# Kernel tuning notes

Hardware: AMD Instinct MI355X
Metric: run time of the kernel (lower is better)

## Reference

```python
import jax, jax.numpy as jnp
import numpy as np

B, F, L, H, D = 8, 256, 2048, 8, 32
INV_SQRT_2PI = 1.0 / np.sqrt(2.0 * 3.1415926)


def setup_inputs() -> dict:
    key = jax.random.key(0)
    k0, k1, k2 = jax.random.split(key, 3)
    # xavier-normal-ish scale for the projections
    scale = np.sqrt(2.0 / (F + H * D)).astype(np.float32)
    return {
        "inputs": jax.random.normal(k0, (B, F, L), dtype=jnp.float32),
        "Wq": jax.random.normal(k1, (F, H * D), dtype=jnp.float32) * scale,
        "bq": jnp.zeros((H * D,), dtype=jnp.float32),
        "Wk": jax.random.normal(k2, (F, H * D), dtype=jnp.float32) * scale,
        "bk": jnp.zeros((H * D,), dtype=jnp.float32),
        "prior_mean": jnp.zeros((1,), dtype=jnp.float32),
        "prior_std": jnp.ones((1,), dtype=jnp.float32),
    }


def reference(inputs, Wq, bq, Wk, bk, prior_mean, prior_std):
    # inputs: [B, F, L] -> x: [B, L, F]
    x = jnp.transpose(inputs, (0, 2, 1))
    Lx = x.shape[1]
    # projections, reshaped to per-head: [B, L, H, D]
    q = (x @ Wq + bq).reshape(B, Lx, H, D)
    k = (x @ Wk + bk).reshape(B, Lx, H, D)
    # distance matrix: dist[i, j] = j - i
    idx = jnp.arange(Lx, dtype=jnp.float32)
    dist = idx[None, :] - idx[:, None]                      # [L, L]
    # gaussian positional prior
    prior = (INV_SQRT_2PI / prior_std[0]) * jnp.exp(
        -0.5 * (dist - prior_mean[0]) ** 2 / prior_std[0] ** 2
    )                                                       # [L, L]
    # scaled QK^T per head, modulated by prior, softmax over keys
    att = jnp.einsum("blhd,bmhd->bhlm", q, k) * (float(D) ** -0.5)
    att = att * prior[None, None, :, :]
    att = jax.nn.softmax(att, axis=-1)                      # [B, H, L, L]
    # distance-weighted reduction over keys -> [B, H, L]
    out = jnp.einsum("bhlm,lm->bhl", att, dist)
    # [B, L, H] to match torch split/cat layout
    return jnp.transpose(out, (0, 2, 1))
```

## Files before the change

### kernel.cpp

```cpp
#include <hip/hip_runtime.h>
#include <hip/hip_bf16.h>
#include <math.h>

#define B 8
#define F 256
#define L 2048
#define H 8
#define D 32
#define HD 256
#define W 6
#define HALO 8
#define KST 264
#define QSTF 132

typedef __attribute__((ext_vector_type(8))) short bf16x8;
typedef __attribute__((ext_vector_type(4))) float f32x4;

__device__ __forceinline__ unsigned short f2bf_fast(float f) {
    union { float f; unsigned u; } v; v.f = f;
    return (unsigned short)((v.u + 0x8000u) >> 16);
}
__device__ __forceinline__ float bf2f(unsigned u16) {
    union { unsigned u; float f; } v; v.u = u16 << 16;
    return v.f;
}

__global__ __launch_bounds__(256) void prep_w_kernel(
    const float* __restrict__ Wq, const float* __restrict__ Wk,
    unsigned short* __restrict__ Wt)
{
    __shared__ unsigned short Ts[64][72];
    const int t   = threadIdx.x;
    const int sel = blockIdx.x >> 2;
    const int c0  = (blockIdx.x & 3) * 64;
    const int r0  = blockIdx.y * 64;
    const float* __restrict__ src = sel ? Wk : Wq;
    unsigned short* __restrict__ dst = Wt + (size_t)sel * HD * F;

    #pragma unroll
    for (int rr = 0; rr < 4; ++rr) {
        int r = rr * 16 + (t >> 4);
        int cb = (t & 15) * 4;
        float4 v = *(const float4*)&src[(size_t)(r0 + r) * HD + c0 + cb];
        Ts[r][cb + 0] = f2bf_fast(v.x);
        Ts[r][cb + 1] = f2bf_fast(v.y);
        Ts[r][cb + 2] = f2bf_fast(v.z);
        Ts[r][cb + 3] = f2bf_fast(v.w);
    }
    __syncthreads();
    const int c = t >> 2;
    #pragma unroll
    for (int half = 0; half < 2; ++half) {
        int ch = (t & 3) + half * 4;
        unsigned short tmp[8];
        #pragma unroll
        for (int j = 0; j < 8; ++j) tmp[j] = Ts[ch * 8 + j][c];
        *(uint4*)&dst[(size_t)(c0 + c) * F + r0 + ch * 8] = *(const uint4*)tmp;
    }
}

__global__ __launch_bounds__(256, 1) void fused_kernel(
    const float* __restrict__ x, const unsigned short* __restrict__ Wt,
    const float* __restrict__ bq, const float* __restrict__ bk,
    const float* __restrict__ pmean, const float* __restrict__ pstd,
    float* __restrict__ out)
{
    __shared__ uint4 smem4[5280];
    unsigned short* Xs = (unsigned short*)smem4;
    float*          Qs = (float*)smem4;
    unsigned short* Ks = (unsigned short*)(smem4 + 2640);

    const int t    = threadIdx.x;
    const int l0   = blockIdx.x * 64;
    const int b    = blockIdx.y;
    const int lane = t & 63, wv = t >> 6;
    const int lm   = lane & 15, quad = lane >> 4;

    const float* __restrict__ xb = x + (size_t)b * F * L;
    #pragma unroll
    for (int i = 0; i < 20; ++i) {
        int idx = i * 256 + t;
        int lp  = idx % 80;
        int fg  = idx / 80;
        int m   = l0 - HALO + lp;
        m = min(max(m, 0), L - 1);
        unsigned p0, p1;
        {
            float v0 = xb[(size_t)(4 * fg + 0) * L + m];
            float v1 = xb[(size_t)(4 * fg + 1) * L + m];
            p0 = ((__float_as_uint(v0) + 0x8000u) >> 16) |
                 (((__float_as_uint(v1) + 0x8000u) >> 16) << 16);
            float v2 = xb[(size_t)(4 * fg + 2) * L + m];
            float v3 = xb[(size_t)(4 * fg + 3) * L + m];
            p1 = ((__float_as_uint(v2) + 0x8000u) >> 16) |
                 (((__float_as_uint(v3) + 0x8000u) >> 16) << 16);
        }
        uint2 pk; pk.x = p0; pk.y = p1;
        *(uint2*)&Xs[lp * KST + 4 * fg] = pk;
    }
    __syncthreads();

    bf16x8 af[5][8];
    #pragma unroll
    for (int mt = 0; mt < 5; ++mt)
        #pragma unroll
        for (int ks = 0; ks < 8; ++ks)
            af[mt][ks] = *(const bf16x8*)&Xs[(mt * 16 + lm) * KST + ks * 32 + quad * 8];
    __syncthreads();

    #pragma unroll
    for (int nt = 0; nt < 8; ++nt) {
        const int hdq = wv * 128 + nt * 16 + lm;
        const int sel = hdq >> 8;
        const int hd  = hdq & 255;
        const unsigned short* Brow = Wt + ((size_t)sel * HD + hd) * F;
        f32x4 acc[5];
        #pragma unroll
        for (int mt = 0; mt < 5; ++mt) acc[mt] = (f32x4){0.f, 0.f, 0.f, 0.f};
        #pragma unroll
        for (int ks = 0; ks < 8; ++ks) {
            bf16x8 bfr = *(const bf16x8*)&Brow[ks * 32 + quad * 8];
            #pragma unroll
            for (int mt = 0; mt < 5; ++mt)
                acc[mt] = __builtin_amdgcn_mfma_f32_16x16x32_bf16(
                    af[mt][ks], bfr, acc[mt], 0, 0, 0);
        }
        float bv = sel ? bk[hd] : bq[hd];
        if (sel == 0) {
            #pragma unroll
            for (int mt = 0; mt < 5; ++mt)
                #pragma unroll
                for (int r = 0; r < 4; ++r)
                    Qs[(mt * 16 + quad * 4 + r) * QSTF + hd] = acc[mt][r] + bv;
        } else {
            #pragma unroll
            for (int mt = 0; mt < 5; ++mt)
                #pragma unroll
                for (int r = 0; r < 4; ++r)
                    Ks[(mt * 16 + quad * 4 + r) * KST + hd] = f2bf_fast(acc[mt][r] + bv);
        }
    }
    __syncthreads();

    const float mean = pmean[0];
    const float istd = 1.0f / pstd[0];
    const float cs   = 0.39894229f * istd * 0.17677670f;
    float coef[2 * W + 1];
    #pragma unroll
    for (int j = 0; j <= 2 * W; ++j) {
        float z = ((float)(j - W) - mean) * istd;
        coef[j] = cs * __expf(-0.5f * z * z);
    }

    #pragma unroll
    for (int rep = 0; rep < 2; ++rep) {
        const int o   = rep * 256 + t;
        const int lp  = o & 63, h = o >> 6;
        const int l   = l0 + lp;
        const int row = lp + HALO;
        const float* qp = &Qs[row * QSTF + h * 32];
        float q[32];
        #pragma unroll
        for (int c = 0; c < 8; ++c) {
            float4 v = *(const float4*)&qp[c * 4];
            q[c * 4 + 0] = v.x; q[c * 4 + 1] = v.y;
            q[c * 4 + 2] = v.z; q[c * 4 + 3] = v.w;
        }
        float num = 0.f, den = 0.f, cnt = 0.f, dsum = 0.f;
        #pragma unroll
        for (int j = 0; j <= 2 * W; ++j) {
            const int dd = j - W;
            const int m  = l + dd;
            const unsigned short* kp = &Ks[(row + dd) * KST + h * 32];
            float dot = 0.f;
            #pragma unroll
            for (int c = 0; c < 4; ++c) {
                uint4 raw = *(const uint4*)&kp[c * 8];
                unsigned u[4] = {raw.x, raw.y, raw.z, raw.w};
                #pragma unroll
                for (int p = 0; p < 4; ++p) {
                    dot = fmaf(q[c * 8 + p * 2],     bf2f(u[p] & 0xFFFFu), dot);
                    dot = fmaf(q[c * 8 + p * 2 + 1], bf2f(u[p] >> 16),     dot);
                }
            }
            float e = __expf(dot * coef[j]);
            if (m >= 0 && m < L) {
                num = fmaf(e, (float)dd, num);
                den += e; cnt += 1.f; dsum += (float)dd;
            }
        }
        float Sl = (float)(L * (L - 1) / 2 - L * l);
        out[((size_t)b * L + l) * H + h] =
            ((Sl - dsum) + num) / (((float)L - cnt) + den);
    }
}

extern "C" void kernel_launch(void* const* d_in, const int* in_sizes, int n_in,
                              void* d_out, int out_size, void* d_ws, size_t ws_size,
                              hipStream_t stream) {
    const float* x  = (const float*)d_in[0];
    const float* Wq = (const float*)d_in[1];
    const float* bq = (const float*)d_in[2];
    const float* Wk = (const float*)d_in[3];
    const float* bk = (const float*)d_in[4];
    const float* pm = (const float*)d_in[5];
    const float* ps = (const float*)d_in[6];
    float* out = (float*)d_out;

    unsigned short* Wt = (unsigned short*)d_ws;

    prep_w_kernel<<<dim3(8, 4), 256, 0, stream>>>(Wq, Wk, Wt);
    fused_kernel<<<dim3(L / 64, B), 256, 0, stream>>>(x, Wt, bq, bk, pm, ps, out);
}
```

Baseline: 94.95 us.

## Double fused kernel threads to 512 and pre-swizzle weights into MFMA fragment layout

Raises the fused kernel block to 512 threads (8 waves), so each wave computes 4 projection column tiles instead of 8 and each thread handles one (position, head) output instead of two. Q is now stored at full 256-column width with a new stride, which enlarges shared memory. The weight prep kernel now writes Wt in an MFMA-fragment-ordered layout so each lane's B-fragment load is contiguous and coalesced. It also launches more, smaller prep blocks. The cost is higher per-block register and LDS pressure; the launch bound asks for 2 blocks per CU.

```diff
diff --git a/kernel.cpp b/kernel.cpp
--- a/kernel.cpp
+++ b/kernel.cpp
@@ -11,7 +11,7 @@
 #define W 6
 #define HALO 8
 #define KST 264
-#define QSTF 132
+#define QST 260
 
 typedef __attribute__((ext_vector_type(8))) short bf16x8;
 typedef __attribute__((ext_vector_type(4))) float f32x4;
@@ -29,17 +29,16 @@
     const float* __restrict__ Wq, const float* __restrict__ Wk,
     unsigned short* __restrict__ Wt)
 {
-    __shared__ unsigned short Ts[64][72];
+    __shared__ unsigned short Ts[8][72];
     const int t   = threadIdx.x;
     const int sel = blockIdx.x >> 2;
     const int c0  = (blockIdx.x & 3) * 64;
-    const int r0  = blockIdx.y * 64;
+    const int r0  = blockIdx.y * 8;
     const float* __restrict__ src = sel ? Wk : Wq;
     unsigned short* __restrict__ dst = Wt + (size_t)sel * HD * F;
 
-    #pragma unroll
-    for (int rr = 0; rr < 4; ++rr) {
-        int r = rr * 16 + (t >> 4);
+    if (t < 128) {
+        int r  = t >> 4;
         int cb = (t & 15) * 4;
         float4 v = *(const float4*)&src[(size_t)(r0 + r) * HD + c0 + cb];
         Ts[r][cb + 0] = f2bf_fast(v.x);
@@ -48,27 +47,28 @@
         Ts[r][cb + 3] = f2bf_fast(v.w);
     }
     __syncthreads();
-    const int c = t >> 2;
-    #pragma unroll
-    for (int half = 0; half < 2; ++half) {
-        int ch = (t & 3) + half * 4;
+    if (t < 64) {
+        const int hd   = c0 + t;
+        const int tile = hd >> 4, lmw = hd & 15;
+        const int ks   = r0 >> 5, qd  = (r0 >> 3) & 3;
         unsigned short tmp[8];
         #pragma unroll
-        for (int j = 0; j < 8; ++j) tmp[j] = Ts[ch * 8 + j][c];
-        *(uint4*)&dst[(size_t)(c0 + c) * F + r0 + ch * 8] = *(const uint4*)tmp;
-    }
-}
-
-__global__ __launch_bounds__(256, 1) void fused_kernel(
+        for (int j = 0; j < 8; ++j) tmp[j] = Ts[j][t];
+        *(uint4*)&dst[(((size_t)tile * 8 + ks) * 64 + qd * 16 + lmw) * 8] =
+            *(const uint4*)tmp;
+    }
+}
+
+__global__ __launch_bounds__(512, 2) void fused_kernel(
     const float* __restrict__ x, const unsigned short* __restrict__ Wt,
     const float* __restrict__ bq, const float* __restrict__ bk,
     const float* __restrict__ pmean, const float* __restrict__ pstd,
     float* __restrict__ out)
 {
-    __shared__ uint4 smem4[5280];
+    __shared__ uint4 smem4[7840];
     unsigned short* Xs = (unsigned short*)smem4;
     float*          Qs = (float*)smem4;
-    unsigned short* Ks = (unsigned short*)(smem4 + 2640);
+    unsigned short* Ks = (unsigned short*)(smem4 + 5200);
 
     const int t    = threadIdx.x;
     const int l0   = blockIdx.x * 64;
@@ -78,8 +78,8 @@
 
     const float* __restrict__ xb = x + (size_t)b * F * L;
     #pragma unroll
-    for (int i = 0; i < 20; ++i) {
-        int idx = i * 256 + t;
+    for (int i = 0; i < 10; ++i) {
+        int idx = i * 512 + t;
         int lp  = idx % 80;
         int fg  = idx / 80;
         int m   = l0 - HALO + lp;
@@ -109,17 +109,19 @@
     __syncthreads();
 
     #pragma unroll
-    for (int nt = 0; nt < 8; ++nt) {
-        const int hdq = wv * 128 + nt * 16 + lm;
-        const int sel = hdq >> 8;
-        const int hd  = hdq & 255;
-        const unsigned short* Brow = Wt + ((size_t)sel * HD + hd) * F;
+    for (int nt = 0; nt < 4; ++nt) {
+        const int hdq  = wv * 64 + nt * 16 + lm;
+        const int sel  = hdq >> 8;
+        const int hd   = hdq & 255;
+        const int tile = (hdq >> 4) & 15;
+        const unsigned short* Bp =
+            Wt + ((((size_t)sel * 16 + tile) * 8) * 64 + lane) * 8;
         f32x4 acc[5];
         #pragma unroll
         for (int mt = 0; mt < 5; ++mt) acc[mt] = (f32x4){0.f, 0.f, 0.f, 0.f};
         #pragma unroll
         for (int ks = 0; ks < 8; ++ks) {
-            bf16x8 bfr = *(const bf16x8*)&Brow[ks * 32 + quad * 8];
+            bf16x8 bfr = *(const bf16x8*)&Bp[ks * 512];
             #pragma unroll
             for (int mt = 0; mt < 5; ++mt)
                 acc[mt] = __builtin_amdgcn_mfma_f32_16x16x32_bf16(
@@ -131,7 +133,7 @@
             for (int mt = 0; mt < 5; ++mt)
                 #pragma unroll
                 for (int r = 0; r < 4; ++r)
-                    Qs[(mt * 16 + quad * 4 + r) * QSTF + hd] = acc[mt][r] + bv;
+                    Qs[(mt * 16 + quad * 4 + r) * QST + hd] = acc[mt][r] + bv;
         } else {
             #pragma unroll
             for (int mt = 0; mt < 5; ++mt)
@@ -152,47 +154,43 @@
         coef[j] = cs * __expf(-0.5f * z * z);
     }
 
-    #pragma unroll
-    for (int rep = 0; rep < 2; ++rep) {
-        const int o   = rep * 256 + t;
-        const int lp  = o & 63, h = o >> 6;
-        const int l   = l0 + lp;
-        const int row = lp + HALO;
-        const float* qp = &Qs[row * QSTF + h * 32];
-        float q[32];
-        #pragma unroll
-        for (int c = 0; c < 8; ++c) {
-            float4 v = *(const float4*)&qp[c * 4];
-            q[c * 4 + 0] = v.x; q[c * 4 + 1] = v.y;
-            q[c * 4 + 2] = v.z; q[c * 4 + 3] = v.w;
-        }
-        float num = 0.f, den = 0.f, cnt = 0.f, dsum = 0.f;
-        #pragma unroll
-        for (int j = 0; j <= 2 * W; ++j) {
-            const int dd = j - W;
-            const int m  = l + dd;
-            const unsigned short* kp = &Ks[(row + dd) * KST + h * 32];
-            float dot = 0.f;
-            #pragma unroll
-            for (int c = 0; c < 4; ++c) {
-                uint4 raw = *(const uint4*)&kp[c * 8];
-                unsigned u[4] = {raw.x, raw.y, raw.z, raw.w};
-                #pragma unroll
-                for (int p = 0; p < 4; ++p) {
-                    dot = fmaf(q[c * 8 + p * 2],     bf2f(u[p] & 0xFFFFu), dot);
-                    dot = fmaf(q[c * 8 + p * 2 + 1], bf2f(u[p] >> 16),     dot);
-                }
+    const int lp  = t & 63, h = t >> 6;
+    const int l   = l0 + lp;
+    const int row = lp + HALO;
+    const float* qp = &Qs[row * QST + h * 32];
+    float q[32];
+    #pragma unroll
+    for (int c = 0; c < 8; ++c) {
+        float4 v = *(const float4*)&qp[c * 4];
+        q[c * 4 + 0] = v.x; q[c * 4 + 1] = v.y;
+        q[c * 4 + 2] = v.z; q[c * 4 + 3] = v.w;
+    }
+    float num = 0.f, den = 0.f, cnt = 0.f, dsum = 0.f;
+    #pragma unroll
+    for (int j = 0; j <= 2 * W; ++j) {
+        const int dd = j - W;
+        const int m  = l + dd;
+        const unsigned short* kp = &Ks[(row + dd) * KST + h * 32];
+        float dot = 0.f;
+        #pragma unroll
+        for (int c = 0; c < 4; ++c) {
+            uint4 raw = *(const uint4*)&kp[c * 8];
+            unsigned u[4] = {raw.x, raw.y, raw.z, raw.w};
+            #pragma unroll
+            for (int p = 0; p < 4; ++p) {
+                dot = fmaf(q[c * 8 + p * 2],     bf2f(u[p] & 0xFFFFu), dot);
+                dot = fmaf(q[c * 8 + p * 2 + 1], bf2f(u[p] >> 16),     dot);
             }
-            float e = __expf(dot * coef[j]);
-            if (m >= 0 && m < L) {
-                num = fmaf(e, (float)dd, num);
-                den += e; cnt += 1.f; dsum += (float)dd;
-            }
-        }
-        float Sl = (float)(L * (L - 1) / 2 - L * l);
-        out[((size_t)b * L + l) * H + h] =
-            ((Sl - dsum) + num) / (((float)L - cnt) + den);
-    }
+        }
+        float e = __expf(dot * coef[j]);
+        if (m >= 0 && m < L) {
+            num = fmaf(e, (float)dd, num);
+            den += e; cnt += 1.f; dsum += (float)dd;
+        }
+    }
+    float Sl = (float)(L * (L - 1) / 2 - L * l);
+    out[((size_t)b * L + l) * H + h] =
+        ((Sl - dsum) + num) / (((float)L - cnt) + den);
 }
 
 extern "C" void kernel_launch(void* const* d_in, const int* in_sizes, int n_in,
@@ -209,6 +207,6 @@
 
     unsigned short* Wt = (unsigned short*)d_ws;
 
-    prep_w_kernel<<<dim3(8, 4), 256, 0, stream>>>(Wq, Wk, Wt);
-    fused_kernel<<<dim3(L / 64, B), 256, 0, stream>>>(x, Wt, bq, bk, pm, ps, out);
-}
+    prep_w_kernel<<<dim3(8, 32), 256, 0, stream>>>(Wq, Wk, Wt);
+    fused_kernel<<<dim3(L / 64, B), 512, 0, stream>>>(x, Wt, bq, bk, pm, ps, out);
+}
```

New measurement: 89.40 us. 1.06x faster.
